# Performance work log

Hardware: AMD Instinct MI355X
Metric: run time of the kernel (lower is better)

Reference implementation:

```python
import jax, jax.numpy as jnp
import numpy as np

HEADS = 4
DIM_HEAD = 32
SCALE = DIM_HEAD ** -0.5


def setup_inputs() -> dict:
    key = jax.random.key(0)
    k1, k2, k3 = jax.random.split(key, 3)
    dim, hidden = 256, HEADS * DIM_HEAD
    x = jax.random.normal(k1, (4, dim, 64, 64), dtype=jnp.float32)
    w_qkv = jax.random.normal(k2, (hidden * 3, dim), dtype=jnp.float32) * (dim ** -0.5)
    w_out = jax.random.normal(k3, (dim, hidden), dtype=jnp.float32) * (hidden ** -0.5)
    b_out = jnp.zeros((dim,), dtype=jnp.float32)
    return {"x": x, "w_qkv": w_qkv, "w_out": w_out, "b_out": b_out}


def reference(x, w_qkv, w_out, b_out):
    b, c, h, w = x.shape
    # 1x1 conv (no bias) == channel matmul
    qkv = jnp.einsum('bchw,oc->bohw', x, w_qkv)           # [b, 3*hidden, h, w]
    q, k, v = jnp.split(qkv, 3, axis=1)
    def to_heads(t):
        # [b, heads*d, h, w] -> [b, heads, h*w, d]
        return t.reshape(b, HEADS, DIM_HEAD, h * w).transpose(0, 1, 3, 2)
    q, k, v = to_heads(q) * SCALE, to_heads(k), to_heads(v)
    sim = jnp.einsum('bhid,bhjd->bhij', q, k)             # [b, heads, hw, hw]
    attn = jax.nn.softmax(sim, axis=-1)
    out = jnp.einsum('bhij,bhjd->bhid', attn, v)          # [b, heads, hw, d]
    out = out.transpose(0, 1, 3, 2).reshape(b, HEADS * DIM_HEAD, h, w)
    # output 1x1 conv with bias
    return jnp.einsum('bchw,oc->bohw', out, w_out) + b_out[None, :, None, None]
```

## Files before the change

kernel.cpp:

```cpp
#include <hip/hip_runtime.h>
#include <hip/hip_fp16.h>

#define HEADS 4
#define DH    32
#define HW    4096
#define CIN   256
#define HID   128
#define KSPLIT 2
#define KHALF (HW / KSPLIT)
#define NIT   (KHALF / 64)

using half8    = __attribute__((ext_vector_type(8))) _Float16;
using half4    = __attribute__((ext_vector_type(4))) _Float16;
using half2v   = __attribute__((ext_vector_type(2))) _Float16;
using floatx4  = __attribute__((ext_vector_type(4))) float;
using floatx16 = __attribute__((ext_vector_type(16))) float;
using uint4v   = __attribute__((ext_vector_type(4))) unsigned;

#define SHIFT2 4.328085122666891f
#define WQSCALE 0.25508275947f

static __device__ __forceinline__ unsigned pkr(float a, float b) {
  return __builtin_bit_cast(unsigned, __builtin_amdgcn_cvt_pkrtz(a, b));
}

__global__ __launch_bounds__(256) void qkv_fused(
    const float* __restrict__ w, const float* __restrict__ x,
    _Float16* __restrict__ Qw, _Float16* __restrict__ Kw,
    _Float16* __restrict__ Vtw)
{
  __shared__ float t[64][65];
  __shared__ _Float16 As[64][72];
  __shared__ _Float16 Bs[64][72];
  const int mt = blockIdx.x, nt = blockIdx.y;
  const int b = nt >> 6, p0 = (nt & 63) * 64;
  const int tid = threadIdx.x;
  const int wv = tid >> 6, lane = tid & 63, lm = lane & 15, quad = lane >> 4;
  const float wscale = (mt < 2) ? WQSCALE : 1.0f;

  const float* Ag = w + (size_t)(mt * 64) * CIN;
  const float* xb = x + (size_t)b * CIN * HW + p0;

  floatx4 acc[4] = {{0,0,0,0},{0,0,0,0},{0,0,0,0},{0,0,0,0}};

  for (int kq = 0; kq < 4; ++kq) {
    __syncthreads();
    #pragma unroll
    for (int i = 0; i < 4; ++i) {
      int ci = tid + i * 256;
      int cc = ci >> 4, p4 = (ci & 15) * 4;
      *(float4*)&t[cc][p4] =
          *(const float4*)(xb + (size_t)(kq * 64 + cc) * HW + p4);
    }
    #pragma unroll
    for (int i = 0; i < 2; ++i) {
      int ci = tid + i * 256;
      int r = ci >> 3, c8 = (ci & 7) * 8;
      const float* src = Ag + (size_t)r * CIN + kq * 64 + c8;
      float4 u0 = *(const float4*)(src);
      float4 u1 = *(const float4*)(src + 4);
      half8 h = {(_Float16)(u0.x * wscale), (_Float16)(u0.y * wscale),
                 (_Float16)(u0.z * wscale), (_Float16)(u0.w * wscale),
                 (_Float16)(u1.x * wscale), (_Float16)(u1.y * wscale),
                 (_Float16)(u1.z * wscale), (_Float16)(u1.w * wscale)};
      *(half8*)&As[r][c8] = h;
    }
    __syncthreads();
    #pragma unroll
    for (int i = 0; i < 2; ++i) {
      int idx = tid + i * 256;
      int p = idx >> 3, c0 = (idx & 7) * 8;
      half8 v;
      #pragma unroll
      for (int k = 0; k < 8; ++k) v[k] = (_Float16)t[c0 + k][p];
      *(half8*)&Bs[p][c0] = v;
    }
    __syncthreads();
    #pragma unroll
    for (int ks = 0; ks < 2; ++ks) {
      half8 a = *(const half8*)&As[wv * 16 + lm][ks * 32 + quad * 8];
      #pragma unroll
      for (int ns = 0; ns < 4; ++ns) {
        half8 bf = *(const half8*)&Bs[ns * 16 + lm][ks * 32 + quad * 8];
        acc[ns] = __builtin_amdgcn_mfma_f32_16x16x32_f16(a, bf, acc[ns], 0, 0, 0);
      }
    }
  }

  const int sec = mt >> 1;
  const int o_base = (mt & 1) * 64 + wv * 16 + quad * 4;
  const int hh = o_base >> 5, dd = o_base & 31;
  const int bh = b * HEADS + hh;
  if (sec < 2) {
    _Float16* dst = (sec == 0) ? Qw : Kw;
    #pragma unroll
    for (int ns = 0; ns < 4; ++ns) {
      int p = p0 + ns * 16 + lm;
      half4 v = {(_Float16)acc[ns][0], (_Float16)acc[ns][1],
                 (_Float16)acc[ns][2], (_Float16)acc[ns][3]};
      *(half4*)(dst + ((size_t)bh * HW + p) * DH + dd) = v;
    }
  } else {
    #pragma unroll
    for (int ns = 0; ns < 4; ++ns) {
      int p = p0 + ns * 16 + lm;
      #pragma unroll
      for (int r = 0; r < 4; ++r)
        Vtw[((size_t)bh * DH + dd + r) * HW + p] = (_Float16)acc[ns][r];
    }
  }
}

__global__ __launch_bounds__(256) void attn(
    const _Float16* __restrict__ Qw, const _Float16* __restrict__ Kw,
    const _Float16* __restrict__ Vtw, float* __restrict__ Op,
    float* __restrict__ lp)
{
  __shared__ _Float16 ks[2][64][40];
  __shared__ _Float16 vt[2][32][72];

  const int bh = blockIdx.y, qt = blockIdx.x, z = blockIdx.z;
  const int tid = threadIdx.x;
  const int wv = tid >> 6, lane = tid & 63;
  const int l31 = lane & 31, hi = lane >> 5;

  const _Float16* qbase =
      Qw + ((size_t)bh * HW + qt * 128 + wv * 32 + l31) * DH + hi * 8;
  const half8 qb0 = *(const half8*)qbase;
  const half8 qb1 = *(const half8*)(qbase + 16);

  const floatx16 shift16 = {-SHIFT2,-SHIFT2,-SHIFT2,-SHIFT2,
                            -SHIFT2,-SHIFT2,-SHIFT2,-SHIFT2,
                            -SHIFT2,-SHIFT2,-SHIFT2,-SHIFT2,
                            -SHIFT2,-SHIFT2,-SHIFT2,-SHIFT2};
  floatx16 oT = {0,0,0,0,0,0,0,0,0,0,0,0,0,0,0,0};
  float lsum = 0.0f;

  const _Float16* kbase = Kw  + (size_t)bh * HW * DH + (size_t)z * KHALF * DH;
  const _Float16* vbase = Vtw + (size_t)bh * DH * HW + (size_t)z * KHALF;
  const int kr = tid >> 2, kc = (tid & 3) * 8;
  const int vr = tid >> 3, vc = (tid & 7) * 8;
  const int kwc = (((tid & 3) ^ ((kr >> 3) & 3)) << 3);
  const int vwc = (((tid & 7) ^ ((vr >> 3) & 3)) << 3);
  const int kx = (l31 >> 3) & 3;

  half8 kA = *(const half8*)(kbase + (size_t)kr * DH + kc);
  half8 vA = *(const half8*)(vbase + (size_t)vr * HW + vc);
  *(half8*)&ks[0][kr][kwc] = kA;
  *(half8*)&vt[0][vr][vwc] = vA;
  kA = *(const half8*)(kbase + ((size_t)64 + kr) * DH + kc);
  vA = *(const half8*)(vbase + (size_t)vr * HW + 64 + vc);
  __syncthreads();

  for (int it = 0; it < NIT; ++it) {
    const int ph = it & 1, nx = ph ^ 1;

    half8 ka[2][2];
    half8 va[4];
    #pragma unroll
    for (int t = 0; t < 2; ++t)
      #pragma unroll
      for (int d = 0; d < 2; ++d)
        ka[t][d] = *(const half8*)&ks[ph][t * 32 + l31][((d * 2 + hi) ^ kx) << 3];
    #pragma unroll
    for (int k4 = 0; k4 < 4; ++k4)
      va[k4] = *(const half8*)&vt[ph][l31][((k4 * 2 + hi) ^ kx) << 3];

    *(half8*)&ks[nx][kr][kwc] = kA;
    *(half8*)&vt[nx][vr][vwc] = vA;
    size_t koff = (size_t)(it + 2) * 64;
    if (koff > KHALF - 64) koff = KHALF - 64;
    kA = *(const half8*)(kbase + (koff + kr) * DH + kc);
    vA = *(const half8*)(vbase + (size_t)vr * HW + koff + vc);

    #pragma unroll
    for (int t = 0; t < 2; ++t) {
      floatx16 sT = __builtin_amdgcn_mfma_f32_32x32x16_f16(ka[t][0], qb0, shift16, 0, 0, 0);
      sT = __builtin_amdgcn_mfma_f32_32x32x16_f16(ka[t][1], qb1, sT, 0, 0, 0);
      float e[16];
      #pragma unroll
      for (int r = 0; r < 16; ++r) e[r] = __builtin_amdgcn_exp2f(sT[r]);
      lsum += (((e[0]+e[1])+(e[2]+e[3]))+((e[4]+e[5])+(e[6]+e[7])))
            + (((e[8]+e[9])+(e[10]+e[11]))+((e[12]+e[13])+(e[14]+e[15])));
      unsigned w0 = pkr(e[0],  e[1]),  w1 = pkr(e[2],  e[3]);
      unsigned w2 = pkr(e[4],  e[5]),  w3 = pkr(e[6],  e[7]);
      unsigned w4 = pkr(e[8],  e[9]),  w5 = pkr(e[10], e[11]);
      unsigned w6 = pkr(e[12], e[13]), w7 = pkr(e[14], e[15]);
      asm("v_permlane32_swap_b32 %0, %1" : "+v"(w0), "+v"(w2));
      asm("v_permlane32_swap_b32 %0, %1" : "+v"(w1), "+v"(w3));
      asm("v_permlane32_swap_b32 %0, %1" : "+v"(w4), "+v"(w6));
      asm("v_permlane32_swap_b32 %0, %1" : "+v"(w5), "+v"(w7));
      uint4v lo4 = {w0, w1, w2, w3}, hi4 = {w4, w5, w6, w7};
      half8 pbLo = __builtin_bit_cast(half8, lo4);
      half8 pbHi = __builtin_bit_cast(half8, hi4);
      oT = __builtin_amdgcn_mfma_f32_32x32x16_f16(va[2*t],     pbLo, oT, 0, 0, 0);
      oT = __builtin_amdgcn_mfma_f32_32x32x16_f16(va[2*t + 1], pbHi, oT, 0, 0, 0);
    }
    __syncthreads();
  }

  lsum += __shfl_xor(lsum, 32, 64);
  const int b = bh >> 2, hh = bh & 3;
  const int row = qt * 128 + wv * 32 + l31;
  float* obase = Op + ((size_t)z * 4 * HW + (size_t)b * HW + row) * HID + hh * DH;
  #pragma unroll
  for (int r0 = 0; r0 < 4; ++r0) {
    float4 v = {oT[4*r0], oT[4*r0+1], oT[4*r0+2], oT[4*r0+3]};
    *(float4*)(obase + 8 * r0 + 4 * hi) = v;
  }
  if (lane < 32)
    lp[(size_t)z * HEADS * 4 * HW + (size_t)bh * HW + row] = lsum;
}

__global__ __launch_bounds__(256) void out_gemm(
    const float* __restrict__ wo, const float* __restrict__ Op,
    const float* __restrict__ lp, const float* __restrict__ bo,
    float* __restrict__ out)
{
  __shared__ _Float16 As[64][136];
  __shared__ _Float16 Bs[64][136];
  __shared__ float os[64][68];
  __shared__ float inv_l[64][4];
  const int mt = blockIdx.x, nt = blockIdx.y;
  const int b = nt >> 6, p0 = (nt & 63) * 64;
  const int tid = threadIdx.x;
  const int wv = tid >> 6, lane = tid & 63, lm = lane & 15, quad = lane >> 4;

  {
    const int p = tid >> 2, hh = tid & 3;
    const size_t qi = (size_t)(b * HEADS + hh) * HW + p0 + p;
    inv_l[p][hh] = 1.0f / (lp[qi] + lp[(size_t)HEADS * 4 * HW + qi]);
  }
  __syncthreads();

  const float* Ag  = wo + (size_t)(mt * 64) * HID;
  const float* Bp0 = Op + ((size_t)b * HW + p0) * HID;
  const float* Bp1 = Bp0 + (size_t)4 * HW * HID;

  #pragma unroll
  for (int i = 0; i < 4; ++i) {
    int ci = tid + i * 256;
    int r = ci >> 4, c8 = (ci & 15) * 8;
    const float* src = Ag + (size_t)r * HID + c8;
    float4 u0 = *(const float4*)(src);
    float4 u1 = *(const float4*)(src + 4);
    half8 h = {(_Float16)u0.x, (_Float16)u0.y, (_Float16)u0.z, (_Float16)u0.w,
               (_Float16)u1.x, (_Float16)u1.y, (_Float16)u1.z, (_Float16)u1.w};
    *(half8*)&As[r][c8] = h;

    const float* s0 = Bp0 + (size_t)r * HID + c8;
    const float* s1 = Bp1 + (size_t)r * HID + c8;
    float4 o0 = *(const float4*)(s0);
    float4 o1 = *(const float4*)(s0 + 4);
    float4 o2 = *(const float4*)(s1);
    float4 o3 = *(const float4*)(s1 + 4);
    const float sc = inv_l[r][c8 >> 5];
    half8 hb = {(_Float16)((o0.x + o2.x) * sc), (_Float16)((o0.y + o2.y) * sc),
                (_Float16)((o0.z + o2.z) * sc), (_Float16)((o0.w + o2.w) * sc),
                (_Float16)((o1.x + o3.x) * sc), (_Float16)((o1.y + o3.y) * sc),
                (_Float16)((o1.z + o3.z) * sc), (_Float16)((o1.w + o3.w) * sc)};
    *(half8*)&Bs[r][c8] = hb;
  }
  __syncthreads();

  floatx4 acc[4] = {{0,0,0,0},{0,0,0,0},{0,0,0,0},{0,0,0,0}};
  #pragma unroll
  for (int ks = 0; ks < 4; ++ks) {
    half8 a = *(const half8*)&As[wv * 16 + lm][ks * 32 + quad * 8];
    #pragma unroll
    for (int ns = 0; ns < 4; ++ns) {
      half8 bf = *(const half8*)&Bs[ns * 16 + lm][ks * 32 + quad * 8];
      acc[ns] = __builtin_amdgcn_mfma_f32_16x16x32_f16(a, bf, acc[ns], 0, 0, 0);
    }
  }

  #pragma unroll
  for (int ns = 0; ns < 4; ++ns)
    #pragma unroll
    for (int r = 0; r < 4; ++r)
      os[wv * 16 + quad * 4 + r][ns * 16 + lm] = acc[ns][r];
  __syncthreads();

  const int o = tid >> 2, pq = (tid & 3) * 16;
  const float bias = bo[mt * 64 + o];
  float* dst = out + ((size_t)(b * CIN + mt * 64 + o)) * HW + p0 + pq;
  #pragma unroll
  for (int j = 0; j < 4; ++j) {
    float4 v = *(const float4*)&os[o][pq + j * 4];
    v.x += bias; v.y += bias; v.z += bias; v.w += bias;
    *(float4*)(dst + j * 4) = v;
  }
}

extern "C" void kernel_launch(void* const* d_in, const int* in_sizes, int n_in,
                              void* d_out, int out_size, void* d_ws, size_t ws_size,
                              hipStream_t stream)
{
  const float* x     = (const float*)d_in[0];
  const float* w_qkv = (const float*)d_in[1];
  const float* w_out = (const float*)d_in[2];
  const float* b_out = (const float*)d_in[3];
  float* out = (float*)d_out;

  char* ws = (char*)d_ws;
  _Float16* Qw  = (_Float16*)(ws);
  _Float16* Kw  = (_Float16*)(ws + (4u  << 20));
  _Float16* Vtw = (_Float16*)(ws + (8u  << 20));
  float*    Op  = (float*)   (ws + (12u << 20));
  float*    lp  = (float*)   (ws + (28u << 20));

  dim3 blk(256);
  qkv_fused<<<dim3(6, 256), blk, 0, stream>>>(w_qkv, x, Qw, Kw, Vtw);
  attn<<<dim3(32, 16, KSPLIT), blk, 0, stream>>>(Qw, Kw, Vtw, Op, lp);
  out_gemm<<<dim3(4, 256), blk, 0, stream>>>(w_out, Op, lp, b_out, out);
}
```

Before: 161.8 us.

## Reuse staged activation tiles across multiple weight tiles in QKV and output GEMMs

Each qkv_fused block now computes three 64-row output tiles and reuses one transposed x tile for all of them, so the grid shrinks from 6 to 2 along M. out_gemm likewise computes two output tiles per block from a single normalized Op tile, and writes results straight from the accumulators instead of staging them through shared memory. The aim is to stop re-reading and re-converting x and Op for every output tile. In exchange there are fewer blocks, more accumulator registers, extra barriers per weight tile, and less coalesced direct stores in out_gemm.

```diff
diff --git a/kernel.cpp b/kernel.cpp
--- a/kernel.cpp
+++ b/kernel.cpp
@@ -32,16 +32,16 @@
   __shared__ float t[64][65];
   __shared__ _Float16 As[64][72];
   __shared__ _Float16 Bs[64][72];
-  const int mt = blockIdx.x, nt = blockIdx.y;
+  const int mg = blockIdx.x, nt = blockIdx.y;
   const int b = nt >> 6, p0 = (nt & 63) * 64;
   const int tid = threadIdx.x;
   const int wv = tid >> 6, lane = tid & 63, lm = lane & 15, quad = lane >> 4;
-  const float wscale = (mt < 2) ? WQSCALE : 1.0f;
-
-  const float* Ag = w + (size_t)(mt * 64) * CIN;
+
   const float* xb = x + (size_t)b * CIN * HW + p0;
 
-  floatx4 acc[4] = {{0,0,0,0},{0,0,0,0},{0,0,0,0},{0,0,0,0}};
+  floatx4 acc[3][4] = {{{0,0,0,0},{0,0,0,0},{0,0,0,0},{0,0,0,0}},
+                       {{0,0,0,0},{0,0,0,0},{0,0,0,0},{0,0,0,0}},
+                       {{0,0,0,0},{0,0,0,0},{0,0,0,0},{0,0,0,0}}};
 
   for (int kq = 0; kq < 4; ++kq) {
     __syncthreads();
@@ -52,19 +52,6 @@
       *(float4*)&t[cc][p4] =
           *(const float4*)(xb + (size_t)(kq * 64 + cc) * HW + p4);
     }
-    #pragma unroll
-    for (int i = 0; i < 2; ++i) {
-      int ci = tid + i * 256;
-      int r = ci >> 3, c8 = (ci & 7) * 8;
-      const float* src = Ag + (size_t)r * CIN + kq * 64 + c8;
-      float4 u0 = *(const float4*)(src);
-      float4 u1 = *(const float4*)(src + 4);
-      half8 h = {(_Float16)(u0.x * wscale), (_Float16)(u0.y * wscale),
-                 (_Float16)(u0.z * wscale), (_Float16)(u0.w * wscale),
-                 (_Float16)(u1.x * wscale), (_Float16)(u1.y * wscale),
-                 (_Float16)(u1.z * wscale), (_Float16)(u1.w * wscale)};
-      *(half8*)&As[r][c8] = h;
-    }
     __syncthreads();
     #pragma unroll
     for (int i = 0; i < 2; ++i) {
@@ -75,38 +62,63 @@
       for (int k = 0; k < 8; ++k) v[k] = (_Float16)t[c0 + k][p];
       *(half8*)&Bs[p][c0] = v;
     }
-    __syncthreads();
-    #pragma unroll
-    for (int ks = 0; ks < 2; ++ks) {
-      half8 a = *(const half8*)&As[wv * 16 + lm][ks * 32 + quad * 8];
+
+    #pragma unroll
+    for (int im = 0; im < 3; ++im) {
+      const int mt = mg * 3 + im;
+      const float wscale = (mt < 2) ? WQSCALE : 1.0f;
+      const float* Ag = w + (size_t)(mt * 64) * CIN;
+      __syncthreads();
+      #pragma unroll
+      for (int i = 0; i < 2; ++i) {
+        int ci = tid + i * 256;
+        int r = ci >> 3, c8 = (ci & 7) * 8;
+        const float* src = Ag + (size_t)r * CIN + kq * 64 + c8;
+        float4 u0 = *(const float4*)(src);
+        float4 u1 = *(const float4*)(src + 4);
+        half8 h = {(_Float16)(u0.x * wscale), (_Float16)(u0.y * wscale),
+                   (_Float16)(u0.z * wscale), (_Float16)(u0.w * wscale),
+                   (_Float16)(u1.x * wscale), (_Float16)(u1.y * wscale),
+                   (_Float16)(u1.z * wscale), (_Float16)(u1.w * wscale)};
+        *(half8*)&As[r][c8] = h;
+      }
+      __syncthreads();
+      #pragma unroll
+      for (int ks = 0; ks < 2; ++ks) {
+        half8 a = *(const half8*)&As[wv * 16 + lm][ks * 32 + quad * 8];
+        #pragma unroll
+        for (int ns = 0; ns < 4; ++ns) {
+          half8 bf = *(const half8*)&Bs[ns * 16 + lm][ks * 32 + quad * 8];
+          acc[im][ns] = __builtin_amdgcn_mfma_f32_16x16x32_f16(a, bf, acc[im][ns], 0, 0, 0);
+        }
+      }
+    }
+  }
+
+  #pragma unroll
+  for (int im = 0; im < 3; ++im) {
+    const int mt = mg * 3 + im;
+    const int sec = mt >> 1;
+    const int o_base = (mt & 1) * 64 + wv * 16 + quad * 4;
+    const int hh = o_base >> 5, dd = o_base & 31;
+    const int bh = b * HEADS + hh;
+    if (sec < 2) {
+      _Float16* dst = (sec == 0) ? Qw : Kw;
       #pragma unroll
       for (int ns = 0; ns < 4; ++ns) {
-        half8 bf = *(const half8*)&Bs[ns * 16 + lm][ks * 32 + quad * 8];
-        acc[ns] = __builtin_amdgcn_mfma_f32_16x16x32_f16(a, bf, acc[ns], 0, 0, 0);
-      }
-    }
-  }
-
-  const int sec = mt >> 1;
-  const int o_base = (mt & 1) * 64 + wv * 16 + quad * 4;
-  const int hh = o_base >> 5, dd = o_base & 31;
-  const int bh = b * HEADS + hh;
-  if (sec < 2) {
-    _Float16* dst = (sec == 0) ? Qw : Kw;
-    #pragma unroll
-    for (int ns = 0; ns < 4; ++ns) {
-      int p = p0 + ns * 16 + lm;
-      half4 v = {(_Float16)acc[ns][0], (_Float16)acc[ns][1],
-                 (_Float16)acc[ns][2], (_Float16)acc[ns][3]};
-      *(half4*)(dst + ((size_t)bh * HW + p) * DH + dd) = v;
-    }
-  } else {
-    #pragma unroll
-    for (int ns = 0; ns < 4; ++ns) {
-      int p = p0 + ns * 16 + lm;
-      #pragma unroll
-      for (int r = 0; r < 4; ++r)
-        Vtw[((size_t)bh * DH + dd + r) * HW + p] = (_Float16)acc[ns][r];
+        int p = p0 + ns * 16 + lm;
+        half4 v = {(_Float16)acc[im][ns][0], (_Float16)acc[im][ns][1],
+                   (_Float16)acc[im][ns][2], (_Float16)acc[im][ns][3]};
+        *(half4*)(dst + ((size_t)bh * HW + p) * DH + dd) = v;
+      }
+    } else {
+      #pragma unroll
+      for (int ns = 0; ns < 4; ++ns) {
+        int p = p0 + ns * 16 + lm;
+        #pragma unroll
+        for (int r = 0; r < 4; ++r)
+          Vtw[((size_t)bh * DH + dd + r) * HW + p] = (_Float16)acc[im][ns][r];
+      }
     }
   }
 }
@@ -219,9 +231,8 @@
 {
   __shared__ _Float16 As[64][136];
   __shared__ _Float16 Bs[64][136];
-  __shared__ float os[64][68];
   __shared__ float inv_l[64][4];
-  const int mt = blockIdx.x, nt = blockIdx.y;
+  const int mg = blockIdx.x, nt = blockIdx.y;
   const int b = nt >> 6, p0 = (nt & 63) * 64;
   const int tid = threadIdx.x;
   const int wv = tid >> 6, lane = tid & 63, lm = lane & 15, quad = lane >> 4;
@@ -233,7 +244,6 @@
   }
   __syncthreads();
 
-  const float* Ag  = wo + (size_t)(mt * 64) * HID;
   const float* Bp0 = Op + ((size_t)b * HW + p0) * HID;
   const float* Bp1 = Bp0 + (size_t)4 * HW * HID;
 
@@ -241,13 +251,6 @@
   for (int i = 0; i < 4; ++i) {
     int ci = tid + i * 256;
     int r = ci >> 4, c8 = (ci & 15) * 8;
-    const float* src = Ag + (size_t)r * HID + c8;
-    float4 u0 = *(const float4*)(src);
-    float4 u1 = *(const float4*)(src + 4);
-    half8 h = {(_Float16)u0.x, (_Float16)u0.y, (_Float16)u0.z, (_Float16)u0.w,
-               (_Float16)u1.x, (_Float16)u1.y, (_Float16)u1.z, (_Float16)u1.w};
-    *(half8*)&As[r][c8] = h;
-
     const float* s0 = Bp0 + (size_t)r * HID + c8;
     const float* s1 = Bp1 + (size_t)r * HID + c8;
     float4 o0 = *(const float4*)(s0);
@@ -261,34 +264,46 @@
                 (_Float16)((o1.z + o3.z) * sc), (_Float16)((o1.w + o3.w) * sc)};
     *(half8*)&Bs[r][c8] = hb;
   }
-  __syncthreads();
-
-  floatx4 acc[4] = {{0,0,0,0},{0,0,0,0},{0,0,0,0},{0,0,0,0}};
+
   #pragma unroll
-  for (int ks = 0; ks < 4; ++ks) {
-    half8 a = *(const half8*)&As[wv * 16 + lm][ks * 32 + quad * 8];
-    #pragma unroll
-    for (int ns = 0; ns < 4; ++ns) {
-      half8 bf = *(const half8*)&Bs[ns * 16 + lm][ks * 32 + quad * 8];
-      acc[ns] = __builtin_amdgcn_mfma_f32_16x16x32_f16(a, bf, acc[ns], 0, 0, 0);
-    }
-  }
-
-  #pragma unroll
-  for (int ns = 0; ns < 4; ++ns)
-    #pragma unroll
-    for (int r = 0; r < 4; ++r)
-      os[wv * 16 + quad * 4 + r][ns * 16 + lm] = acc[ns][r];
-  __syncthreads();
-
-  const int o = tid >> 2, pq = (tid & 3) * 16;
-  const float bias = bo[mt * 64 + o];
-  float* dst = out + ((size_t)(b * CIN + mt * 64 + o)) * HW + p0 + pq;
-  #pragma unroll
-  for (int j = 0; j < 4; ++j) {
-    float4 v = *(const float4*)&os[o][pq + j * 4];
-    v.x += bias; v.y += bias; v.z += bias; v.w += bias;
-    *(float4*)(dst + j * 4) = v;
+  for (int im = 0; im < 2; ++im) {
+    const int mt = mg * 2 + im;
+    const float* Ag = wo + (size_t)(mt * 64) * HID;
+    __syncthreads();
+    #pragma unroll
+    for (int i = 0; i < 4; ++i) {
+      int ci = tid + i * 256;
+      int r = ci >> 4, c8 = (ci & 15) * 8;
+      const float* src = Ag + (size_t)r * HID + c8;
+      float4 u0 = *(const float4*)(src);
+      float4 u1 = *(const float4*)(src + 4);
+      half8 h = {(_Float16)u0.x, (_Float16)u0.y, (_Float16)u0.z, (_Float16)u0.w,
+                 (_Float16)u1.x, (_Float16)u1.y, (_Float16)u1.z, (_Float16)u1.w};
+      *(half8*)&As[r][c8] = h;
+    }
+    __syncthreads();
+
+    floatx4 acc[4] = {{0,0,0,0},{0,0,0,0},{0,0,0,0},{0,0,0,0}};
+    #pragma unroll
+    for (int ks = 0; ks < 4; ++ks) {
+      half8 a = *(const half8*)&As[wv * 16 + lm][ks * 32 + quad * 8];
+      #pragma unroll
+      for (int ns = 0; ns < 4; ++ns) {
+        half8 bf = *(const half8*)&Bs[ns * 16 + lm][ks * 32 + quad * 8];
+        acc[ns] = __builtin_amdgcn_mfma_f32_16x16x32_f16(a, bf, acc[ns], 0, 0, 0);
+      }
+    }
+
+    const int o_loc = wv * 16 + quad * 4;
+    #pragma unroll
+    for (int r = 0; r < 4; ++r) {
+      const int o = mt * 64 + o_loc + r;
+      const float bias = bo[o];
+      float* dst = out + ((size_t)(b * CIN + o)) * HW + p0 + lm;
+      #pragma unroll
+      for (int ns = 0; ns < 4; ++ns)
+        dst[ns * 16] = acc[ns][r] + bias;
+    }
   }
 }
 
@@ -310,7 +325,7 @@
   float*    lp  = (float*)   (ws + (28u << 20));
 
   dim3 blk(256);
-  qkv_fused<<<dim3(6, 256), blk, 0, stream>>>(w_qkv, x, Qw, Kw, Vtw);
+  qkv_fused<<<dim3(2, 256), blk, 0, stream>>>(w_qkv, x, Qw, Kw, Vtw);
   attn<<<dim3(32, 16, KSPLIT), blk, 0, stream>>>(Qw, Kw, Vtw, Op, lp);
-  out_gemm<<<dim3(4, 256), blk, 0, stream>>>(w_out, Op, lp, b_out, out);
-}
+  out_gemm<<<dim3(2, 256), blk, 0, stream>>>(w_out, Op, lp, b_out, out);
+}
```

After: 157.3 us. 2.8% less time.
